# Optimization experiments

Hardware: AMD Instinct MI355X
Metric: run time of the kernel (lower is better)

Reference implementation:

```python
import jax, jax.numpy as jnp
import numpy as np

N_NODES = 50000
N_EDGES = 800000
N_GRAPHS = 512
F_IN = 9
H = 64
H2 = 32


def gcn_conv(x, W, b, edge_index, num_nodes):
    # PyG GCNConv: add self loops, sym-normalize, x @ W, scatter-add, + bias
    src, dst = edge_index[0], edge_index[1]
    xw = x @ W  # [N, out]
    deg = 1.0 + jax.ops.segment_sum(jnp.ones_like(src, dtype=xw.dtype), dst,
                                    num_segments=num_nodes)  # self-loop adds 1
    dis = jax.lax.rsqrt(deg)  # deg >= 1
    norm = dis[src] * dis[dst]  # [E]
    out = jax.ops.segment_sum(xw[src] * norm[:, None], dst, num_segments=num_nodes)
    out = out + xw * (dis * dis)[:, None]  # self-loop contribution
    return out + b


def edge_conv(x, W, b, edge_index, num_nodes):
    # PyG EdgeConv with nn = Linear(2*in, out) + ReLU, aggr='max'
    src, dst = edge_index[0], edge_index[1]
    xi = x[dst]
    xj = x[src]
    h = jax.nn.relu(jnp.concatenate([xi, xj - xi], axis=-1) @ W + b)  # [E, out]
    agg = jax.ops.segment_max(h, dst, num_segments=num_nodes)
    return jnp.where(jnp.isfinite(agg), agg, 0.0)  # empty segments -> 0


def setup_inputs() -> dict:
    key = jax.random.key(0)
    ks = jax.random.split(key, 16)
    x = jax.random.normal(ks[0], (N_NODES, F_IN), dtype=jnp.float32)
    edge_index = jax.random.randint(ks[1], (2, N_EDGES), 0, N_NODES, dtype=jnp.int32)
    adj = jax.random.randint(ks[2], (2, N_EDGES), 0, N_NODES, dtype=jnp.int32)
    batch = jnp.sort(jax.random.randint(ks[3], (N_NODES,), 0, N_GRAPHS, dtype=jnp.int32))
    s = lambda fan_in: 1.0 / np.sqrt(fan_in)
    W1 = jax.random.uniform(ks[4], (F_IN, H), jnp.float32, -s(F_IN), s(F_IN))
    b1 = jnp.zeros((H,), jnp.float32)
    eW1 = jax.random.uniform(ks[5], (2 * H, H), jnp.float32, -s(2 * H), s(2 * H))
    eb1 = jnp.zeros((H,), jnp.float32)
    W2 = jax.random.uniform(ks[6], (H, H2), jnp.float32, -s(H), s(H))
    b2 = jnp.zeros((H2,), jnp.float32)
    eW2 = jax.random.uniform(ks[7], (2 * H2, H2), jnp.float32, -s(2 * H2), s(2 * H2))
    eb2 = jnp.zeros((H2,), jnp.float32)
    fcW = jax.random.uniform(ks[8], (H2, 1), jnp.float32, -s(H2), s(H2))
    fcb = jax.random.uniform(ks[9], (1,), jnp.float32, -s(H2), s(H2))
    return {"x": x, "edge_index": edge_index, "adj": adj, "batch": batch,
            "W1": W1, "b1": b1, "eW1": eW1, "eb1": eb1,
            "W2": W2, "b2": b2, "eW2": eW2, "eb2": eb2,
            "fcW": fcW, "fcb": fcb}


def reference(x, edge_index, adj, batch, W1, b1, eW1, eb1, W2, b2, eW2, eb2, fcW, fcb):
    n = x.shape[0]
    h = jax.nn.relu(gcn_conv(x, W1, b1, edge_index, n))
    h = jax.nn.relu(edge_conv(h, eW1, eb1, adj, n))
    h = jax.nn.relu(gcn_conv(h, W2, b2, edge_index, n))
    h = jax.nn.relu(edge_conv(h, eW2, eb2, adj, n))
    h = h @ fcW + fcb  # [N, 1]
    # global_mean_pool
    sums = jax.ops.segment_sum(h, batch, num_segments=N_GRAPHS)
    cnts = jax.ops.segment_sum(jnp.ones((n, 1), h.dtype), batch, num_segments=N_GRAPHS)
    return sums / jnp.maximum(cnts, 1.0)
```

## Files before the change

kernel.cpp:

```cpp
#include <hip/hip_runtime.h>
#include <math.h>

#define NN 50000
#define NE 800000
#define NG 512
#define FIN 9
#define D1 64
#define D2 32
#define NN2 (2 * NN)

static inline int cdiv(int a, int b) { return (a + b - 1) / b; }

__global__ void k_build(const int* __restrict__ ei, const int* __restrict__ adj,
                        int* __restrict__ head_e, int* __restrict__ next_e,
                        int* __restrict__ head_a, int* __restrict__ next_a) {
  int e = blockIdx.x * blockDim.x + threadIdx.x;
  if (e < NE) {
    int d1 = ei[NE + e];
    next_e[e] = atomicExch(&head_e[d1], e);
    int d2 = adj[NE + e];
    next_a[e] = atomicExch(&head_a[d2], e);
  }
}

__global__ void k_count(const int* __restrict__ head_e, const int* __restrict__ next_e,
                        const int* __restrict__ head_a, const int* __restrict__ next_a,
                        int* __restrict__ deg, float* __restrict__ dis) {
  int t = blockIdx.x * blockDim.x + threadIdx.x;
  if (t >= NN2) return;
  bool isE = t < NN;
  int e = isE ? head_e[t] : head_a[t - NN];
  const int* nxt = isE ? next_e : next_a;
  int c = 0;
  while (e >= 0) {
    ++c;
    e = nxt[e];
  }
  deg[t] = c;
  if (isE) dis[t] = rsqrtf(1.0f + (float)c);
}

__global__ void k_scan_a(const int* __restrict__ deg, int* __restrict__ off,
                         int* __restrict__ partial) {
  __shared__ int tmp[256];
  int i = blockIdx.x * 256 + threadIdx.x;
  int v = (i < NN2) ? deg[i] : 0;
  tmp[threadIdx.x] = v;
  __syncthreads();
  for (int d = 1; d < 256; d <<= 1) {
    int t = (threadIdx.x >= d) ? tmp[threadIdx.x - d] : 0;
    __syncthreads();
    tmp[threadIdx.x] += t;
    __syncthreads();
  }
  if (i < NN2) off[i] = tmp[threadIdx.x] - v;
  if (threadIdx.x == 255) partial[blockIdx.x] = tmp[255];
}

__global__ void k_scan_b(int* __restrict__ partial, int nb) {
  __shared__ int tmp[512];
  int v = (threadIdx.x < nb) ? partial[threadIdx.x] : 0;
  tmp[threadIdx.x] = v;
  __syncthreads();
  for (int d = 1; d < 512; d <<= 1) {
    int t = (threadIdx.x >= d) ? tmp[threadIdx.x - d] : 0;
    __syncthreads();
    tmp[threadIdx.x] += t;
    __syncthreads();
  }
  if (threadIdx.x < nb) partial[threadIdx.x] = tmp[threadIdx.x] - v;
}

__global__ void k_scan_c(int* __restrict__ off, const int* __restrict__ partial) {
  int i = blockIdx.x * 256 + threadIdx.x;
  if (i < NN2) off[i] += partial[blockIdx.x];
  if (i == 0) off[NN2] = 2 * NE;
}

__global__ void k_convert(const int* __restrict__ head_e, const int* __restrict__ next_e,
                          const int* __restrict__ head_a, const int* __restrict__ next_a,
                          const int* __restrict__ ei, const int* __restrict__ adj,
                          const int* __restrict__ off, int* __restrict__ srcbuf) {
  int t = blockIdx.x * blockDim.x + threadIdx.x;
  if (t >= NN2) return;
  bool isE = t < NN;
  int e = isE ? head_e[t] : head_a[t - NN];
  const int* nxt = isE ? next_e : next_a;
  const int* sv = isE ? ei : adj;
  int pos = off[t];
  while (e >= 0) {
    srcbuf[pos++] = sv[e];
    e = nxt[e];
  }
}

__global__ void k_xw1(const float* __restrict__ x, const float* __restrict__ W1,
                      const float* __restrict__ dis, float* __restrict__ xws1) {
  int gid = blockIdx.x * blockDim.x + threadIdx.x;
  int i = gid >> 6, j = gid & 63;
  if (i >= NN) return;
  const float* xr = x + i * FIN;
  float acc = 0.f;
#pragma unroll
  for (int k = 0; k < FIN; ++k) acc += xr[k] * W1[k * D1 + j];
  xws1[i * D1 + j] = acc * dis[i];
}

template <int FI, int FOT, int MODE, bool SCALE>
__global__ __launch_bounds__(256) void k_gemm(const float* __restrict__ H,
                                              const float* __restrict__ W,
                                              const float* __restrict__ dis,
                                              float* __restrict__ OA,
                                              float* __restrict__ OB) {
  constexpr int TM = 4;
  constexpr int TN = (FOT >= 64) ? 4 : 2;
  constexpr int BN = 1024 * TN / FOT;
  constexpr int LDH = BN + 1;
  constexpr int FO = FOT / 2;
  __shared__ float ht[FI][LDH];
  __shared__ float wc[FI][FOT];

  for (int t = threadIdx.x; t < FI * FOT; t += 256) {
    int k = t / FOT, j = t % FOT;
    float v;
    if (MODE == 1)
      v = (j < FO) ? W[k * FO + j] : W[(FI + k) * FO + (j - FO)];
    else
      v = W[k * FOT + j];
    wc[k][j] = v;
  }
  int node0 = blockIdx.x * BN;
  for (int t = threadIdx.x; t < BN * FI; t += 256) {
    int n = t / FI, k = t % FI;
    int nn = node0 + n;
    ht[k][n] = (nn < NN) ? H[(size_t)nn * FI + k] : 0.f;
  }
  __syncthreads();

  int tn = threadIdx.x % (FOT / TN);
  int tm = threadIdx.x / (FOT / TN);
  int j0 = tn * TN, n0 = tm * TM;

  float acc[TM][TN];
#pragma unroll
  for (int m = 0; m < TM; ++m)
#pragma unroll
    for (int q = 0; q < TN; ++q) acc[m][q] = 0.f;

  for (int k = 0; k < FI; ++k) {
    float wv[TN];
    if (TN == 4) {
      float4 w4 = *(const float4*)&wc[k][j0];
      wv[0] = w4.x; wv[1] = w4.y; wv[2] = w4.z; wv[3] = w4.w;
    } else {
      float2 w2 = *(const float2*)&wc[k][j0];
      wv[0] = w2.x; wv[1] = w2.y;
    }
    float hv[TM];
#pragma unroll
    for (int m = 0; m < TM; ++m) hv[m] = ht[k][n0 + m];
#pragma unroll
    for (int m = 0; m < TM; ++m)
#pragma unroll
      for (int q = 0; q < TN; ++q) acc[m][q] += hv[m] * wv[q];
  }

#pragma unroll
  for (int m = 0; m < TM; ++m) {
    int n = node0 + n0 + m;
    if (n >= NN) break;
    float sc = SCALE ? dis[n] : 1.0f;
    float* dst;
    if (MODE == 1)
      dst = (j0 < FO) ? (OA + (size_t)n * FO + j0) : (OB + (size_t)n * FO + (j0 - FO));
    else
      dst = OA + (size_t)n * FOT + j0;
    if (TN == 4) {
      float4 o = {acc[m][0] * sc, acc[m][1] * sc, acc[m][2] * sc, acc[m][3] * sc};
      *(float4*)dst = o;
    } else {
      float2 o = {acc[m][0] * sc, acc[m][1] * sc};
      *(float2*)dst = o;
    }
  }
}

template <int F>
__global__ void k_gcn(const float* __restrict__ xws, const float* __restrict__ dis,
                      const int* __restrict__ off, const int* __restrict__ srcs,
                      const float* __restrict__ b, float* __restrict__ hout) {
  int gid = blockIdx.x * blockDim.x + threadIdx.x;
  int i = gid / F, j = gid % F;
  if (i >= NN) return;
  float acc = xws[(size_t)i * F + j];
  int s = off[i], e = off[i + 1];
  int t = s;
  for (; t + 3 < e; t += 4) {
    int s0 = srcs[t], s1 = srcs[t + 1], s2 = srcs[t + 2], s3 = srcs[t + 3];
    float v0 = xws[(size_t)s0 * F + j];
    float v1 = xws[(size_t)s1 * F + j];
    float v2 = xws[(size_t)s2 * F + j];
    float v3 = xws[(size_t)s3 * F + j];
    acc += v0 + v1 + v2 + v3;
  }
  for (; t < e; ++t) acc += xws[(size_t)srcs[t] * F + j];
  float o = b[j] + dis[i] * acc;
  hout[(size_t)i * F + j] = fmaxf(o, 0.f);
}

template <int F>
__global__ void k_edge(const float* __restrict__ A, const float* __restrict__ B,
                       const float* __restrict__ eb, const int* __restrict__ off,
                       const int* __restrict__ srcs, float* __restrict__ hout) {
  int gid = blockIdx.x * blockDim.x + threadIdx.x;
  int i = gid / F, j = gid % F;
  if (i >= NN) return;
  float M = -INFINITY;
  int s = off[i], e = off[i + 1];
  int t = s;
  for (; t + 3 < e; t += 4) {
    int s0 = srcs[t], s1 = srcs[t + 1], s2 = srcs[t + 2], s3 = srcs[t + 3];
    float v0 = B[(size_t)s0 * F + j];
    float v1 = B[(size_t)s1 * F + j];
    float v2 = B[(size_t)s2 * F + j];
    float v3 = B[(size_t)s3 * F + j];
    M = fmaxf(M, fmaxf(fmaxf(v0, v1), fmaxf(v2, v3)));
  }
  for (; t < e; ++t) M = fmaxf(M, B[(size_t)srcs[t] * F + j]);
  float base = A[(size_t)i * F + j] - B[(size_t)i * F + j] + eb[j];
  hout[(size_t)i * F + j] = fmaxf(base + M, 0.f);
}

__global__ void k_final(const float* __restrict__ h4, const float* __restrict__ fcW,
                        const float* __restrict__ fcb, const int* __restrict__ batch,
                        float* __restrict__ sums, float* __restrict__ cnt) {
  int i = blockIdx.x * blockDim.x + threadIdx.x;
  int lane = threadIdx.x & 63;
  bool valid = (i < NN);
  float val = 0.f, c = 0.f;
  int g = -1;
  if (valid) {
    float acc = fcb[0];
#pragma unroll
    for (int k = 0; k < D2; ++k) acc += h4[(size_t)i * D2 + k] * fcW[k];
    val = acc;
    c = 1.f;
    g = batch[i];
  }
#pragma unroll
  for (int d = 1; d < 64; d <<= 1) {
    float v2 = __shfl_down(val, d);
    float c2 = __shfl_down(c, d);
    int g2 = __shfl_down(g, d);
    if (lane + d < 64 && g2 == g) {
      val += v2;
      c += c2;
    }
  }
  int gprev = __shfl_up(g, 1);
  bool is_head = (lane == 0) || (gprev != g);
  if (valid && is_head) {
    atomicAdd(&sums[g], val);
    atomicAdd(&cnt[g], c);
  }
}

__global__ void k_out(const float* __restrict__ sums, const float* __restrict__ cnt,
                      float* __restrict__ out) {
  int g = blockIdx.x * blockDim.x + threadIdx.x;
  if (g < NG) out[g] = sums[g] / fmaxf(cnt[g], 1.0f);
}

extern "C" void kernel_launch(void* const* d_in, const int* in_sizes, int n_in,
                              void* d_out, int out_size, void* d_ws, size_t ws_size,
                              hipStream_t stream) {
  const float* x = (const float*)d_in[0];
  const int* ei = (const int*)d_in[1];
  const int* adj = (const int*)d_in[2];
  const int* batch = (const int*)d_in[3];
  const float* W1 = (const float*)d_in[4];
  const float* b1 = (const float*)d_in[5];
  const float* eW1 = (const float*)d_in[6];
  const float* eb1 = (const float*)d_in[7];
  const float* W2 = (const float*)d_in[8];
  const float* b2 = (const float*)d_in[9];
  const float* eW2 = (const float*)d_in[10];
  const float* eb2 = (const float*)d_in[11];
  const float* fcW = (const float*)d_in[12];
  const float* fcb = (const float*)d_in[13];
  float* out = (float*)d_out;

  char* ws = (char*)d_ws;
  size_t p = 0;
  auto alloc = [&](size_t bytes) -> void* {
    void* r = ws + p;
    p = (p + bytes + 255) & ~(size_t)255;
    return r;
  };
  int* head_e = (int*)alloc(NN * 4);
  int* head_a = (int*)alloc(NN * 4);
  size_t ff_bytes = p;
  float* sums = (float*)alloc(NG * 4);
  float* cnt = (float*)alloc(NG * 4);
  size_t zero_end = p;
  int* next_e = (int*)alloc(NE * 4);
  int* next_a = (int*)alloc(NE * 4);
  int* deg = (int*)alloc(NN2 * 4);
  int* off = (int*)alloc((NN2 + 1) * 4);
  int* part = (int*)alloc(512 * 4);
  int* srcbuf = (int*)alloc((size_t)2 * NE * 4);
  float* dis = (float*)alloc(NN * 4);
  float* buf0 = (float*)alloc((size_t)NN * D1 * 4);
  float* buf1 = (float*)alloc((size_t)NN * D1 * 4);
  float* buf2 = (float*)alloc((size_t)NN * D1 * 4);
  float* buf3 = (float*)alloc((size_t)NN * D1 * 4);

  const int NBS = cdiv(NN2, 256);

  hipMemsetAsync(d_ws, 0xFF, ff_bytes, stream);
  hipMemsetAsync(ws + ff_bytes, 0, zero_end - ff_bytes, stream);

  k_build<<<cdiv(NE, 256), 256, 0, stream>>>(ei, adj, head_e, next_e, head_a, next_a);
  k_count<<<NBS, 256, 0, stream>>>(head_e, next_e, head_a, next_a, deg, dis);
  k_scan_a<<<NBS, 256, 0, stream>>>(deg, off, part);
  k_scan_b<<<1, 512, 0, stream>>>(part, NBS);
  k_scan_c<<<NBS, 256, 0, stream>>>(off, part);
  k_convert<<<NBS, 256, 0, stream>>>(head_e, next_e, head_a, next_a, ei, adj, off, srcbuf);

  k_xw1<<<cdiv(NN * D1, 256), 256, 0, stream>>>(x, W1, dis, buf0);
  k_gcn<D1><<<cdiv(NN * D1, 256), 256, 0, stream>>>(buf0, dis, off, srcbuf, b1, buf1);

  k_gemm<D1, 2 * D1, 1, false><<<cdiv(NN, 32), 256, 0, stream>>>(buf1, eW1, nullptr, buf2, buf3);
  k_edge<D1><<<cdiv(NN * D1, 256), 256, 0, stream>>>(buf2, buf3, eb1, off + NN, srcbuf, buf0);

  k_gemm<D1, D2, 0, true><<<cdiv(NN, 64), 256, 0, stream>>>(buf0, W2, dis, buf1, nullptr);
  k_gcn<D2><<<cdiv(NN * D2, 256), 256, 0, stream>>>(buf1, dis, off, srcbuf, b2, buf3);

  float* A2 = buf2;
  float* B2 = buf2 + (size_t)NN * D2;
  k_gemm<D2, 2 * D2, 1, false><<<cdiv(NN, 64), 256, 0, stream>>>(buf3, eW2, nullptr, A2, B2);
  k_edge<D2><<<cdiv(NN * D2, 256), 256, 0, stream>>>(A2, B2, eb2, off + NN, srcbuf, buf1);

  k_final<<<cdiv(NN, 256), 256, 0, stream>>>(buf1, fcW, fcb, batch, sums, cnt);
  k_out<<<cdiv(NG, 256), 256, 0, stream>>>(sums, cnt, out);
}
```

Measured before the change: 439.2 us.

## Replace three-pass scan with wave-level atomic offsets and vectorize gather kernels

Removes the three prefix-scan kernels. Each wave now does a shuffle scan of the node degrees and takes a base offset from a global atomic cursor, so neighbour lists are laid out in a non-sorted but contiguous order, and the end of each segment is computed as off+deg. The GCN and EdgeConv gather kernels now process four features per thread with float4 loads, which cuts the number of threads and gives wider memory transactions for the random-row gathers. In exchange, segment order depends on how waves are scheduled, so float summation order can vary between runs.

```diff
diff --git a/kernel.cpp b/kernel.cpp
--- a/kernel.cpp
+++ b/kernel.cpp
@@ -25,56 +25,36 @@
 
 __global__ void k_count(const int* __restrict__ head_e, const int* __restrict__ next_e,
                         const int* __restrict__ head_a, const int* __restrict__ next_a,
-                        int* __restrict__ deg, float* __restrict__ dis) {
+                        int* __restrict__ deg, int* __restrict__ off,
+                        int* __restrict__ cursor, float* __restrict__ dis) {
   int t = blockIdx.x * blockDim.x + threadIdx.x;
-  if (t >= NN2) return;
-  bool isE = t < NN;
-  int e = isE ? head_e[t] : head_a[t - NN];
-  const int* nxt = isE ? next_e : next_a;
+  int lane = threadIdx.x & 63;
+  bool valid = (t < NN2);
   int c = 0;
-  while (e >= 0) {
-    ++c;
-    e = nxt[e];
-  }
-  deg[t] = c;
-  if (isE) dis[t] = rsqrtf(1.0f + (float)c);
-}
-
-__global__ void k_scan_a(const int* __restrict__ deg, int* __restrict__ off,
-                         int* __restrict__ partial) {
-  __shared__ int tmp[256];
-  int i = blockIdx.x * 256 + threadIdx.x;
-  int v = (i < NN2) ? deg[i] : 0;
-  tmp[threadIdx.x] = v;
-  __syncthreads();
-  for (int d = 1; d < 256; d <<= 1) {
-    int t = (threadIdx.x >= d) ? tmp[threadIdx.x - d] : 0;
-    __syncthreads();
-    tmp[threadIdx.x] += t;
-    __syncthreads();
-  }
-  if (i < NN2) off[i] = tmp[threadIdx.x] - v;
-  if (threadIdx.x == 255) partial[blockIdx.x] = tmp[255];
-}
-
-__global__ void k_scan_b(int* __restrict__ partial, int nb) {
-  __shared__ int tmp[512];
-  int v = (threadIdx.x < nb) ? partial[threadIdx.x] : 0;
-  tmp[threadIdx.x] = v;
-  __syncthreads();
-  for (int d = 1; d < 512; d <<= 1) {
-    int t = (threadIdx.x >= d) ? tmp[threadIdx.x - d] : 0;
-    __syncthreads();
-    tmp[threadIdx.x] += t;
-    __syncthreads();
-  }
-  if (threadIdx.x < nb) partial[threadIdx.x] = tmp[threadIdx.x] - v;
-}
-
-__global__ void k_scan_c(int* __restrict__ off, const int* __restrict__ partial) {
-  int i = blockIdx.x * 256 + threadIdx.x;
-  if (i < NN2) off[i] += partial[blockIdx.x];
-  if (i == 0) off[NN2] = 2 * NE;
+  if (valid) {
+    bool isE = t < NN;
+    int e = isE ? head_e[t] : head_a[t - NN];
+    const int* nxt = isE ? next_e : next_a;
+    while (e >= 0) {
+      ++c;
+      e = nxt[e];
+    }
+  }
+  int sc = c;
+#pragma unroll
+  for (int d = 1; d < 64; d <<= 1) {
+    int v = __shfl_up(sc, d);
+    if (lane >= d) sc += v;
+  }
+  int total = __shfl(sc, 63);
+  int base = 0;
+  if (lane == 63) base = atomicAdd(cursor, total);
+  base = __shfl(base, 63);
+  if (valid) {
+    deg[t] = c;
+    off[t] = base + sc - c;
+    if (t < NN) dis[t] = rsqrtf(1.0f + (float)c);
+  }
 }
 
 __global__ void k_convert(const int* __restrict__ head_e, const int* __restrict__ next_e,
@@ -186,49 +166,79 @@
 }
 
 template <int F>
-__global__ void k_gcn(const float* __restrict__ xws, const float* __restrict__ dis,
-                      const int* __restrict__ off, const int* __restrict__ srcs,
-                      const float* __restrict__ b, float* __restrict__ hout) {
+__global__ void k_gcn4(const float4* __restrict__ xws, const float* __restrict__ dis,
+                       const int* __restrict__ off, const int* __restrict__ deg,
+                       const int* __restrict__ srcs, const float* __restrict__ b,
+                       float4* __restrict__ hout) {
+  constexpr int L = F / 4;
   int gid = blockIdx.x * blockDim.x + threadIdx.x;
-  int i = gid / F, j = gid % F;
+  int i = gid / L, l = gid % L;
   if (i >= NN) return;
-  float acc = xws[(size_t)i * F + j];
-  int s = off[i], e = off[i + 1];
+  float4 acc = xws[(size_t)i * L + l];
+  int s = off[i], e = s + deg[i];
   int t = s;
   for (; t + 3 < e; t += 4) {
     int s0 = srcs[t], s1 = srcs[t + 1], s2 = srcs[t + 2], s3 = srcs[t + 3];
-    float v0 = xws[(size_t)s0 * F + j];
-    float v1 = xws[(size_t)s1 * F + j];
-    float v2 = xws[(size_t)s2 * F + j];
-    float v3 = xws[(size_t)s3 * F + j];
-    acc += v0 + v1 + v2 + v3;
-  }
-  for (; t < e; ++t) acc += xws[(size_t)srcs[t] * F + j];
-  float o = b[j] + dis[i] * acc;
-  hout[(size_t)i * F + j] = fmaxf(o, 0.f);
+    float4 v0 = xws[(size_t)s0 * L + l];
+    float4 v1 = xws[(size_t)s1 * L + l];
+    float4 v2 = xws[(size_t)s2 * L + l];
+    float4 v3 = xws[(size_t)s3 * L + l];
+    acc.x += (v0.x + v1.x) + (v2.x + v3.x);
+    acc.y += (v0.y + v1.y) + (v2.y + v3.y);
+    acc.z += (v0.z + v1.z) + (v2.z + v3.z);
+    acc.w += (v0.w + v1.w) + (v2.w + v3.w);
+  }
+  for (; t < e; ++t) {
+    float4 v = xws[(size_t)srcs[t] * L + l];
+    acc.x += v.x; acc.y += v.y; acc.z += v.z; acc.w += v.w;
+  }
+  float di = dis[i];
+  float4 bb = ((const float4*)b)[l];
+  float4 o;
+  o.x = fmaxf(bb.x + di * acc.x, 0.f);
+  o.y = fmaxf(bb.y + di * acc.y, 0.f);
+  o.z = fmaxf(bb.z + di * acc.z, 0.f);
+  o.w = fmaxf(bb.w + di * acc.w, 0.f);
+  hout[(size_t)i * L + l] = o;
 }
 
 template <int F>
-__global__ void k_edge(const float* __restrict__ A, const float* __restrict__ B,
-                       const float* __restrict__ eb, const int* __restrict__ off,
-                       const int* __restrict__ srcs, float* __restrict__ hout) {
+__global__ void k_edge4(const float4* __restrict__ A, const float4* __restrict__ B,
+                        const float* __restrict__ eb, const int* __restrict__ off,
+                        const int* __restrict__ deg, const int* __restrict__ srcs,
+                        float4* __restrict__ hout) {
+  constexpr int L = F / 4;
   int gid = blockIdx.x * blockDim.x + threadIdx.x;
-  int i = gid / F, j = gid % F;
+  int i = gid / L, l = gid % L;
   if (i >= NN) return;
-  float M = -INFINITY;
-  int s = off[i], e = off[i + 1];
+  float4 M = {-INFINITY, -INFINITY, -INFINITY, -INFINITY};
+  int s = off[i], e = s + deg[i];
   int t = s;
   for (; t + 3 < e; t += 4) {
     int s0 = srcs[t], s1 = srcs[t + 1], s2 = srcs[t + 2], s3 = srcs[t + 3];
-    float v0 = B[(size_t)s0 * F + j];
-    float v1 = B[(size_t)s1 * F + j];
-    float v2 = B[(size_t)s2 * F + j];
-    float v3 = B[(size_t)s3 * F + j];
-    M = fmaxf(M, fmaxf(fmaxf(v0, v1), fmaxf(v2, v3)));
-  }
-  for (; t < e; ++t) M = fmaxf(M, B[(size_t)srcs[t] * F + j]);
-  float base = A[(size_t)i * F + j] - B[(size_t)i * F + j] + eb[j];
-  hout[(size_t)i * F + j] = fmaxf(base + M, 0.f);
+    float4 v0 = B[(size_t)s0 * L + l];
+    float4 v1 = B[(size_t)s1 * L + l];
+    float4 v2 = B[(size_t)s2 * L + l];
+    float4 v3 = B[(size_t)s3 * L + l];
+    M.x = fmaxf(M.x, fmaxf(fmaxf(v0.x, v1.x), fmaxf(v2.x, v3.x)));
+    M.y = fmaxf(M.y, fmaxf(fmaxf(v0.y, v1.y), fmaxf(v2.y, v3.y)));
+    M.z = fmaxf(M.z, fmaxf(fmaxf(v0.z, v1.z), fmaxf(v2.z, v3.z)));
+    M.w = fmaxf(M.w, fmaxf(fmaxf(v0.w, v1.w), fmaxf(v2.w, v3.w)));
+  }
+  for (; t < e; ++t) {
+    float4 v = B[(size_t)srcs[t] * L + l];
+    M.x = fmaxf(M.x, v.x); M.y = fmaxf(M.y, v.y);
+    M.z = fmaxf(M.z, v.z); M.w = fmaxf(M.w, v.w);
+  }
+  float4 a = A[(size_t)i * L + l];
+  float4 bsl = B[(size_t)i * L + l];
+  float4 e4 = ((const float4*)eb)[l];
+  float4 o;
+  o.x = fmaxf(a.x - bsl.x + e4.x + M.x, 0.f);
+  o.y = fmaxf(a.y - bsl.y + e4.y + M.y, 0.f);
+  o.z = fmaxf(a.z - bsl.z + e4.z + M.z, 0.f);
+  o.w = fmaxf(a.w - bsl.w + e4.w + M.w, 0.f);
+  hout[(size_t)i * L + l] = o;
 }
 
 __global__ void k_final(const float* __restrict__ h4, const float* __restrict__ fcW,
@@ -302,12 +312,12 @@
   size_t ff_bytes = p;
   float* sums = (float*)alloc(NG * 4);
   float* cnt = (float*)alloc(NG * 4);
+  int* cursor = (int*)alloc(4);
   size_t zero_end = p;
   int* next_e = (int*)alloc(NE * 4);
   int* next_a = (int*)alloc(NE * 4);
   int* deg = (int*)alloc(NN2 * 4);
-  int* off = (int*)alloc((NN2 + 1) * 4);
-  int* part = (int*)alloc(512 * 4);
+  int* off = (int*)alloc(NN2 * 4);
   int* srcbuf = (int*)alloc((size_t)2 * NE * 4);
   float* dis = (float*)alloc(NN * 4);
   float* buf0 = (float*)alloc((size_t)NN * D1 * 4);
@@ -321,25 +331,26 @@
   hipMemsetAsync(ws + ff_bytes, 0, zero_end - ff_bytes, stream);
 
   k_build<<<cdiv(NE, 256), 256, 0, stream>>>(ei, adj, head_e, next_e, head_a, next_a);
-  k_count<<<NBS, 256, 0, stream>>>(head_e, next_e, head_a, next_a, deg, dis);
-  k_scan_a<<<NBS, 256, 0, stream>>>(deg, off, part);
-  k_scan_b<<<1, 512, 0, stream>>>(part, NBS);
-  k_scan_c<<<NBS, 256, 0, stream>>>(off, part);
+  k_count<<<NBS, 256, 0, stream>>>(head_e, next_e, head_a, next_a, deg, off, cursor, dis);
   k_convert<<<NBS, 256, 0, stream>>>(head_e, next_e, head_a, next_a, ei, adj, off, srcbuf);
 
   k_xw1<<<cdiv(NN * D1, 256), 256, 0, stream>>>(x, W1, dis, buf0);
-  k_gcn<D1><<<cdiv(NN * D1, 256), 256, 0, stream>>>(buf0, dis, off, srcbuf, b1, buf1);
+  k_gcn4<D1><<<cdiv(NN * (D1 / 4), 256), 256, 0, stream>>>(
+      (const float4*)buf0, dis, off, deg, srcbuf, b1, (float4*)buf1);
 
   k_gemm<D1, 2 * D1, 1, false><<<cdiv(NN, 32), 256, 0, stream>>>(buf1, eW1, nullptr, buf2, buf3);
-  k_edge<D1><<<cdiv(NN * D1, 256), 256, 0, stream>>>(buf2, buf3, eb1, off + NN, srcbuf, buf0);
+  k_edge4<D1><<<cdiv(NN * (D1 / 4), 256), 256, 0, stream>>>(
+      (const float4*)buf2, (const float4*)buf3, eb1, off + NN, deg + NN, srcbuf, (float4*)buf0);
 
   k_gemm<D1, D2, 0, true><<<cdiv(NN, 64), 256, 0, stream>>>(buf0, W2, dis, buf1, nullptr);
-  k_gcn<D2><<<cdiv(NN * D2, 256), 256, 0, stream>>>(buf1, dis, off, srcbuf, b2, buf3);
+  k_gcn4<D2><<<cdiv(NN * (D2 / 4), 256), 256, 0, stream>>>(
+      (const float4*)buf1, dis, off, deg, srcbuf, b2, (float4*)buf3);
 
   float* A2 = buf2;
   float* B2 = buf2 + (size_t)NN * D2;
   k_gemm<D2, 2 * D2, 1, false><<<cdiv(NN, 64), 256, 0, stream>>>(buf3, eW2, nullptr, A2, B2);
-  k_edge<D2><<<cdiv(NN * D2, 256), 256, 0, stream>>>(A2, B2, eb2, off + NN, srcbuf, buf1);
+  k_edge4<D2><<<cdiv(NN * (D2 / 4), 256), 256, 0, stream>>>(
+      (const float4*)A2, (const float4*)B2, eb2, off + NN, deg + NN, srcbuf, (float4*)buf1);
 
   k_final<<<cdiv(NN, 256), 256, 0, stream>>>(buf1, fcW, fcb, batch, sums, cnt);
   k_out<<<cdiv(NG, 256), 256, 0, stream>>>(sums, cnt, out);
```

New measurement: 411.0 us. 6.4% less time.
